# Kernel tuning notes

Measured on AMD Instinct MI355X. Metric: run time of the kernel, lower is better.

## Reference

```python
import jax, jax.numpy as jnp
import numpy as np

B, S, HQ, HKV, D = 2, 1024, 32, 8, 128

def setup_inputs() -> dict:
    key = jax.random.key(0)
    k1, k2, k3 = jax.random.split(key, 3)
    xq = jax.random.normal(k1, (B, S, HQ, D), dtype=jnp.float32)
    xk = jax.random.normal(k2, (B, S, HKV, D), dtype=jnp.float32)
    xv = jax.random.normal(k3, (B, S, HKV, D), dtype=jnp.float32)
    kv_buffer = jnp.zeros((B * S, 2 * HKV, D), dtype=jnp.float32)
    cur_select_index = jnp.arange(B * S, dtype=jnp.int64 if jax.config.read('jax_enable_x64') else jnp.int32)
    return {"xq": xq, "xk": xk, "xv": xv, "kv_buffer": kv_buffer,
            "cur_select_index": cur_select_index}


def reference(xq, xk, xv, kv_buffer, cur_select_index):
    b, s, hq, d = xq.shape
    hkv = xk.shape[2]
    group = hq // hkv

    # --- KV-cache scatter write: kv_buffer[cur_select_index] = cat(k, v) ---
    combined_kv = jnp.concatenate([xk, xv], axis=2).reshape(-1, 2 * hkv, d)
    kv_buffer_new = kv_buffer.at[cur_select_index].set(combined_kv)

    # --- causal flash-style prefill attention (GQA: repeat kv heads) ---
    scale = 1.0 / np.sqrt(d).astype(np.float32)
    k = jnp.repeat(xk, group, axis=2)  # [b, s, hq, d]
    v = jnp.repeat(xv, group, axis=2)

    scores = jnp.einsum('bqhd,bkhd->bhqk', xq, k) * scale  # [b, hq, s, s]
    causal = jnp.tril(jnp.ones((s, s), dtype=bool))
    scores = jnp.where(causal[None, None], scores, jnp.finfo(scores.dtype).min)
    attn = jax.nn.softmax(scores, axis=-1)
    out = jnp.einsum('bhqk,bkhd->bqhd', attn, v)  # [b, s, hq, d]
    out = out.reshape(b, s, hq * d)
    return out, kv_buffer_new
```

## Files before the change

### kernel.cpp

```cpp
#include <hip/hip_runtime.h>
#include <math.h>

#define B_  2
#define S_  1024
#define HQ_ 32
#define HKV_ 8
#define D_  128

typedef __bf16 bf16x8 __attribute__((ext_vector_type(8)));
typedef float  floatx4 __attribute__((ext_vector_type(4)));

static __device__ __forceinline__ unsigned pack2(float hi, float lo) {
    return __builtin_amdgcn_perm(__float_as_uint(hi), __float_as_uint(lo), 0x07060302u);
}

__global__ void kv_scatter_kernel(const float* __restrict__ xk,
                                  const float* __restrict__ xv,
                                  const int* __restrict__ sel,
                                  float* __restrict__ kv_out) {
    const int total = B_ * S_ * 2 * HKV_ * D_ / 4;
    for (int g = blockIdx.x * 256 + threadIdx.x; g < total; g += gridDim.x * 256) {
        const int t      = g >> 9;
        const int within = g & 511;
        const int idx    = sel[t];
        const float4* src = (within < 256)
            ? ((const float4*)(xk + (size_t)t * (HKV_ * D_)) + within)
            : ((const float4*)(xv + (size_t)t * (HKV_ * D_)) + (within - 256));
        ((float4*)(kv_out + (size_t)idx * (2 * HKV_ * D_)))[within] = *src;
    }
}

__global__ __launch_bounds__(256, 2)
void attn_kernel(const float* __restrict__ xq, const float* __restrict__ xk,
                 const float* __restrict__ xv, float* __restrict__ out) {
    const int b    = blockIdx.z;
    const int qt   = (b == 0) ? (int)blockIdx.x : (31 - (int)blockIdx.x);
    const int hk   = blockIdx.y;
    const int tid  = threadIdx.x;
    const int wave = tid >> 6;
    const int lane = tid & 63;
    const int l15  = lane & 15;
    const int quad = lane >> 4;
    const int L    = lane & 31;
    const int hi32 = lane >> 5;
    const int h    = hk * 4 + wave;

    __shared__ __align__(16) unsigned short Kl[2][32][136];
    __shared__ __align__(16) unsigned int   Vp[2][128][16];
    __shared__ __align__(16) unsigned short Pl[4][16][40];

    bf16x8 qf[2][4];
#pragma unroll
    for (int mt = 0; mt < 2; ++mt) {
        const int row = qt * 32 + mt * 16 + l15;
        const float* qp = xq + (((size_t)(b * S_ + row)) * HQ_ + h) * D_ + quad * 8;
#pragma unroll
        for (int ks = 0; ks < 4; ++ks) {
            union { bf16x8 v; unsigned u[4]; } t2;
            const float4 f0 = *(const float4*)(qp + ks * 32);
            const float4 f1 = *(const float4*)(qp + ks * 32 + 4);
            t2.u[0] = pack2(f0.y, f0.x); t2.u[1] = pack2(f0.w, f0.z);
            t2.u[2] = pack2(f1.y, f1.x); t2.u[3] = pack2(f1.w, f1.z);
            qf[mt][ks] = t2.v;
        }
    }

    bf16x8 ones;
    { union { bf16x8 v; unsigned u[4]; } o;
      o.u[0] = o.u[1] = o.u[2] = o.u[3] = 0x3F803F80u; ones = o.v; }

    floatx4 acc[2][8];
    floatx4 lacc[2];
#pragma unroll
    for (int mt = 0; mt < 2; ++mt) {
        lacc[mt] = (floatx4){0.f, 0.f, 0.f, 0.f};
#pragma unroll
        for (int n = 0; n < 8; ++n) acc[mt][n] = (floatx4){0.f, 0.f, 0.f, 0.f};
    }

    const float scale2 = 0.12751741f;

    float4 pk[4], pv[4];
    const int keyw = wave * 2 + hi32;

    auto loads = [&](int t) {
        const size_t base = ((size_t)(b * S_ + t * 32 + keyw) * HKV_ + hk) * D_ + 4 * L;
#pragma unroll
        for (int i = 0; i < 4; ++i) {
            pk[i] = *(const float4*)(xk + base + (size_t)i * 8 * HKV_ * D_);
            pv[i] = *(const float4*)(xv + base + (size_t)i * 8 * HKV_ * D_);
        }
    };

    auto writesLDS = [&](int bi) {
#pragma unroll
        for (int i = 0; i < 4; ++i) {
            const int key = i * 8 + keyw;
            unsigned kw0 = pack2(pk[i].y, pk[i].x), kw1 = pack2(pk[i].w, pk[i].z);
            *(uint2*)&Kl[bi][key][4 * L] = make_uint2(kw0, kw1);
            unsigned D10 = pack2(pv[i].y, pv[i].x), D32 = pack2(pv[i].w, pv[i].z);
            unsigned P10 = (unsigned)__shfl_xor((int)D10, 32);
            unsigned P32 = (unsigned)__shfl_xor((int)D32, 32);
            unsigned w0 = hi32 ? __builtin_amdgcn_perm(D10, P10, 0x07060302u)
                               : __builtin_amdgcn_perm(P10, D10, 0x05040100u);
            unsigned w2 = hi32 ? __builtin_amdgcn_perm(D32, P32, 0x07060302u)
                               : __builtin_amdgcn_perm(P32, D32, 0x05040100u);
            const int col = 4 * ((i + L) & 3) + wave;
            Vp[bi][4 * L + hi32][col]     = w0;
            Vp[bi][4 * L + hi32 + 2][col] = w2;
        }
    };

    auto compute = [&](int bi, bool lastTile) {
#pragma unroll
        for (int mt = 0; mt < 2; ++mt) {
            floatx4 s0 = (floatx4){0.f, 0.f, 0.f, 0.f};
            floatx4 s1 = (floatx4){0.f, 0.f, 0.f, 0.f};
#pragma unroll
            for (int ks = 0; ks < 4; ++ks) {
                bf16x8 kb0 = *(const bf16x8*)&Kl[bi][l15][ks * 32 + quad * 8];
                bf16x8 kb1 = *(const bf16x8*)&Kl[bi][16 + l15][ks * 32 + quad * 8];
                s0 = __builtin_amdgcn_mfma_f32_16x16x32_bf16(qf[mt][ks], kb0, s0, 0, 0, 0);
                s1 = __builtin_amdgcn_mfma_f32_16x16x32_bf16(qf[mt][ks], kb1, s1, 0, 0, 0);
            }
            float p0[4], p1[4];
            if (lastTile) {
                const int rb = mt * 16 + quad * 4;
#pragma unroll
                for (int r = 0; r < 4; ++r) {
                    p0[r] = (l15      <= rb + r) ? __builtin_amdgcn_exp2f(s0[r] * scale2) : 0.f;
                    p1[r] = (l15 + 16 <= rb + r) ? __builtin_amdgcn_exp2f(s1[r] * scale2) : 0.f;
                }
            } else {
#pragma unroll
                for (int r = 0; r < 4; ++r) {
                    p0[r] = __builtin_amdgcn_exp2f(s0[r] * scale2);
                    p1[r] = __builtin_amdgcn_exp2f(s1[r] * scale2);
                }
            }
#pragma unroll
            for (int r = 0; r < 4; ++r) {
                Pl[wave][quad * 4 + r][l15]      = (unsigned short)(__float_as_uint(p0[r]) >> 16);
                Pl[wave][quad * 4 + r][16 + l15] = (unsigned short)(__float_as_uint(p1[r]) >> 16);
            }
            bf16x8 pa = *(const bf16x8*)&Pl[wave][l15][quad * 8];
            lacc[mt] = __builtin_amdgcn_mfma_f32_16x16x32_bf16(pa, ones, lacc[mt], 0, 0, 0);
#pragma unroll
            for (int n = 0; n < 8; ++n) {
                const int d  = n * 16 + l15;
                const int cb = 4 * ((quad + (d >> 2)) & 3);
                bf16x8 vb = *(const bf16x8*)&Vp[bi][d][cb];
                acc[mt][n] = __builtin_amdgcn_mfma_f32_16x16x32_bf16(pa, vb, acc[mt][n], 0, 0, 0);
            }
        }
    };

    const int nkt = qt + 1;
    loads(0);
    writesLDS(0);
    __syncthreads();
    for (int t = 0; t < nkt; ++t) {
        const int bi = t & 1;
        if (t + 1 < nkt) loads(t + 1);
        compute(bi, t == nkt - 1);
        if (t + 1 < nkt) writesLDS(1 - bi);
        __syncthreads();
    }

#pragma unroll
    for (int mt = 0; mt < 2; ++mt) {
#pragma unroll
        for (int r = 0; r < 4; ++r) {
            const float inv = __builtin_amdgcn_rcpf(lacc[mt][r]);
            const int row = qt * 32 + mt * 16 + quad * 4 + r;
            float* op = out + (((size_t)(b * S_ + row)) * HQ_ + h) * D_ + l15;
#pragma unroll
            for (int n = 0; n < 8; ++n) op[n * 16] = acc[mt][n][r] * inv;
        }
    }
}

extern "C" void kernel_launch(void* const* d_in, const int* in_sizes, int n_in,
                              void* d_out, int out_size, void* d_ws, size_t ws_size,
                              hipStream_t stream) {
    const float* xq  = (const float*)d_in[0];
    const float* xk  = (const float*)d_in[1];
    const float* xv  = (const float*)d_in[2];
    const int*   sel = (const int*)d_in[4];

    float* out    = (float*)d_out;
    float* kv_out = out + (size_t)B_ * S_ * HQ_ * D_;

    kv_scatter_kernel<<<dim3(512), dim3(256), 0, stream>>>(xk, xv, sel, kv_out);
    attn_kernel<<<dim3(32, 8, 2), dim3(256), 0, stream>>>(xq, xk, xv, out);
}
```

Measured before the change: 148.0 us.

## Fuse KV scatter into attention launch and split query rows across eight waves

Merges the KV-cache scatter and the attention kernel into one launch, with the first 128 blocks doing the scatter and the rest doing attention. Attention blocks grow to 512 threads (8 waves), each wave handling one 16-row query slab instead of two, which halves per-wave accumulator registers and the per-thread K/V load work. The intent is to remove a launch and the gap between kernels, raise occupancy, and let the scatter overlap with attention. The cost is that each wave now redoes the QK work on its own 16 rows, and the V LDS swizzle is remapped for eight writer waves.

New measurement: 157.3 us. +6.3%, slower.

```diff
diff --git a/kernel.cpp b/kernel.cpp
--- a/kernel.cpp
+++ b/kernel.cpp
@@ -14,45 +14,55 @@
     return __builtin_amdgcn_perm(__float_as_uint(hi), __float_as_uint(lo), 0x07060302u);
 }
 
-__global__ void kv_scatter_kernel(const float* __restrict__ xk,
-                                  const float* __restrict__ xv,
-                                  const int* __restrict__ sel,
-                                  float* __restrict__ kv_out) {
-    const int total = B_ * S_ * 2 * HKV_ * D_ / 4;
-    for (int g = blockIdx.x * 256 + threadIdx.x; g < total; g += gridDim.x * 256) {
-        const int t      = g >> 9;
-        const int within = g & 511;
-        const int idx    = sel[t];
-        const float4* src = (within < 256)
-            ? ((const float4*)(xk + (size_t)t * (HKV_ * D_)) + within)
-            : ((const float4*)(xv + (size_t)t * (HKV_ * D_)) + (within - 256));
-        ((float4*)(kv_out + (size_t)idx * (2 * HKV_ * D_)))[within] = *src;
+#define SCATTER_BLOCKS 128
+#define ATTN_BLOCKS    512
+
+__global__ __launch_bounds__(512, 4)
+void fused_kernel(const float* __restrict__ xq, const float* __restrict__ xk,
+                  const float* __restrict__ xv, const int* __restrict__ sel,
+                  float* __restrict__ out, float* __restrict__ kv_out) {
+    const int lid = blockIdx.x;
+    const int tid = threadIdx.x;
+
+    if (lid < SCATTER_BLOCKS) {
+        int g = lid * 512 + tid;
+        const int stride = SCATTER_BLOCKS * 512;
+#pragma unroll
+        for (int k = 0; k < 16; ++k, g += stride) {
+            const int t      = g >> 9;
+            const int within = g & 511;
+            const int idx    = sel[t];
+            const float4* src = (within < 256)
+                ? ((const float4*)(xk + (size_t)t * (HKV_ * D_)) + within)
+                : ((const float4*)(xv + (size_t)t * (HKV_ * D_)) + (within - 256));
+            ((float4*)(kv_out + (size_t)idx * (2 * HKV_ * D_)))[within] = *src;
+        }
+        return;
     }
-}
 
-__global__ __launch_bounds__(256, 2)
-void attn_kernel(const float* __restrict__ xq, const float* __restrict__ xk,
-                 const float* __restrict__ xv, float* __restrict__ out) {
-    const int b    = blockIdx.z;
-    const int qt   = (b == 0) ? (int)blockIdx.x : (31 - (int)blockIdx.x);
-    const int hk   = blockIdx.y;
-    const int tid  = threadIdx.x;
+    const int wid = lid - SCATTER_BLOCKS;
+    const int hk  = wid & 7;
+    const int j   = wid >> 3;
+    const int b   = j & 1;
+    const int qq  = j >> 1;
+    const int qt  = b ? (31 - qq) : qq;
+
     const int wave = tid >> 6;
     const int lane = tid & 63;
     const int l15  = lane & 15;
     const int quad = lane >> 4;
     const int L    = lane & 31;
     const int hi32 = lane >> 5;
-    const int h    = hk * 4 + wave;
+    const int h    = hk * 4 + (wave & 3);
+    const int mrow = wave >> 2;
 
     __shared__ __align__(16) unsigned short Kl[2][32][136];
     __shared__ __align__(16) unsigned int   Vp[2][128][16];
-    __shared__ __align__(16) unsigned short Pl[4][16][40];
+    __shared__ __align__(16) unsigned short Pl[8][16][40];
 
-    bf16x8 qf[2][4];
-#pragma unroll
-    for (int mt = 0; mt < 2; ++mt) {
-        const int row = qt * 32 + mt * 16 + l15;
+    bf16x8 qf[4];
+    {
+        const int row = qt * 32 + mrow * 16 + l15;
         const float* qp = xq + (((size_t)(b * S_ + row)) * HQ_ + h) * D_ + quad * 8;
 #pragma unroll
         for (int ks = 0; ks < 4; ++ks) {
@@ -61,7 +71,7 @@
             const float4 f1 = *(const float4*)(qp + ks * 32 + 4);
             t2.u[0] = pack2(f0.y, f0.x); t2.u[1] = pack2(f0.w, f0.z);
             t2.u[2] = pack2(f1.y, f1.x); t2.u[3] = pack2(f1.w, f1.z);
-            qf[mt][ks] = t2.v;
+            qf[ks] = t2.v;
         }
     }
 
@@ -69,33 +79,29 @@
     { union { bf16x8 v; unsigned u[4]; } o;
       o.u[0] = o.u[1] = o.u[2] = o.u[3] = 0x3F803F80u; ones = o.v; }
 
-    floatx4 acc[2][8];
-    floatx4 lacc[2];
+    floatx4 acc[8];
+    floatx4 lacc = (floatx4){0.f, 0.f, 0.f, 0.f};
 #pragma unroll
-    for (int mt = 0; mt < 2; ++mt) {
-        lacc[mt] = (floatx4){0.f, 0.f, 0.f, 0.f};
-#pragma unroll
-        for (int n = 0; n < 8; ++n) acc[mt][n] = (floatx4){0.f, 0.f, 0.f, 0.f};
-    }
+    for (int n = 0; n < 8; ++n) acc[n] = (floatx4){0.f, 0.f, 0.f, 0.f};
 
     const float scale2 = 0.12751741f;
 
-    float4 pk[4], pv[4];
+    float4 pk[2], pv[2];
     const int keyw = wave * 2 + hi32;
 
     auto loads = [&](int t) {
         const size_t base = ((size_t)(b * S_ + t * 32 + keyw) * HKV_ + hk) * D_ + 4 * L;
 #pragma unroll
-        for (int i = 0; i < 4; ++i) {
-            pk[i] = *(const float4*)(xk + base + (size_t)i * 8 * HKV_ * D_);
-            pv[i] = *(const float4*)(xv + base + (size_t)i * 8 * HKV_ * D_);
+        for (int i = 0; i < 2; ++i) {
+            pk[i] = *(const float4*)(xk + base + (size_t)i * 16 * HKV_ * D_);
+            pv[i] = *(const float4*)(xv + base + (size_t)i * 16 * HKV_ * D_);
         }
     };
 
     auto writesLDS = [&](int bi) {
 #pragma unroll
-        for (int i = 0; i < 4; ++i) {
-            const int key = i * 8 + keyw;
+        for (int i = 0; i < 2; ++i) {
+            const int key = i * 16 + keyw;
             unsigned kw0 = pack2(pk[i].y, pk[i].x), kw1 = pack2(pk[i].w, pk[i].z);
             *(uint2*)&Kl[bi][key][4 * L] = make_uint2(kw0, kw1);
             unsigned D10 = pack2(pv[i].y, pv[i].x), D32 = pack2(pv[i].w, pv[i].z);
@@ -105,53 +111,51 @@
                                : __builtin_amdgcn_perm(P10, D10, 0x05040100u);
             unsigned w2 = hi32 ? __builtin_amdgcn_perm(D32, P32, 0x07060302u)
                                : __builtin_amdgcn_perm(P32, D32, 0x05040100u);
-            const int col = 4 * ((i + L) & 3) + wave;
+            const int kp  = i * 8 + wave;
+            const int col = 4 * (((kp >> 2) + L) & 3) + (kp & 3);
             Vp[bi][4 * L + hi32][col]     = w0;
             Vp[bi][4 * L + hi32 + 2][col] = w2;
         }
     };
 
     auto compute = [&](int bi, bool lastTile) {
+        floatx4 s0 = (floatx4){0.f, 0.f, 0.f, 0.f};
+        floatx4 s1 = (floatx4){0.f, 0.f, 0.f, 0.f};
 #pragma unroll
-        for (int mt = 0; mt < 2; ++mt) {
-            floatx4 s0 = (floatx4){0.f, 0.f, 0.f, 0.f};
-            floatx4 s1 = (floatx4){0.f, 0.f, 0.f, 0.f};
-#pragma unroll
-            for (int ks = 0; ks < 4; ++ks) {
-                bf16x8 kb0 = *(const bf16x8*)&Kl[bi][l15][ks * 32 + quad * 8];
-                bf16x8 kb1 = *(const bf16x8*)&Kl[bi][16 + l15][ks * 32 + quad * 8];
-                s0 = __builtin_amdgcn_mfma_f32_16x16x32_bf16(qf[mt][ks], kb0, s0, 0, 0, 0);
-                s1 = __builtin_amdgcn_mfma_f32_16x16x32_bf16(qf[mt][ks], kb1, s1, 0, 0, 0);
-            }
-            float p0[4], p1[4];
-            if (lastTile) {
-                const int rb = mt * 16 + quad * 4;
-#pragma unroll
-                for (int r = 0; r < 4; ++r) {
-                    p0[r] = (l15      <= rb + r) ? __builtin_amdgcn_exp2f(s0[r] * scale2) : 0.f;
-                    p1[r] = (l15 + 16 <= rb + r) ? __builtin_amdgcn_exp2f(s1[r] * scale2) : 0.f;
-                }
-            } else {
-#pragma unroll
-                for (int r = 0; r < 4; ++r) {
-                    p0[r] = __builtin_amdgcn_exp2f(s0[r] * scale2);
-                    p1[r] = __builtin_amdgcn_exp2f(s1[r] * scale2);
-                }
-            }
+        for (int ks = 0; ks < 4; ++ks) {
+            bf16x8 kb0 = *(const bf16x8*)&Kl[bi][l15][ks * 32 + quad * 8];
+            bf16x8 kb1 = *(const bf16x8*)&Kl[bi][16 + l15][ks * 32 + quad * 8];
+            s0 = __builtin_amdgcn_mfma_f32_16x16x32_bf16(qf[ks], kb0, s0, 0, 0, 0);
+            s1 = __builtin_amdgcn_mfma_f32_16x16x32_bf16(qf[ks], kb1, s1, 0, 0, 0);
+        }
+        float p0[4], p1[4];
+        const int rb = mrow * 16 + quad * 4;
+        if (lastTile) {
 #pragma unroll
             for (int r = 0; r < 4; ++r) {
-                Pl[wave][quad * 4 + r][l15]      = (unsigned short)(__float_as_uint(p0[r]) >> 16);
-                Pl[wave][quad * 4 + r][16 + l15] = (unsigned short)(__float_as_uint(p1[r]) >> 16);
+                p0[r] = (l15      <= rb + r) ? __builtin_amdgcn_exp2f(s0[r] * scale2) : 0.f;
+                p1[r] = (l15 + 16 <= rb + r) ? __builtin_amdgcn_exp2f(s1[r] * scale2) : 0.f;
             }
-            bf16x8 pa = *(const bf16x8*)&Pl[wave][l15][quad * 8];
-            lacc[mt] = __builtin_amdgcn_mfma_f32_16x16x32_bf16(pa, ones, lacc[mt], 0, 0, 0);
+        } else {
 #pragma unroll
-            for (int n = 0; n < 8; ++n) {
-                const int d  = n * 16 + l15;
-                const int cb = 4 * ((quad + (d >> 2)) & 3);
-                bf16x8 vb = *(const bf16x8*)&Vp[bi][d][cb];
-                acc[mt][n] = __builtin_amdgcn_mfma_f32_16x16x32_bf16(pa, vb, acc[mt][n], 0, 0, 0);
+            for (int r = 0; r < 4; ++r) {
+                p0[r] = __builtin_amdgcn_exp2f(s0[r] * scale2);
+                p1[r] = __builtin_amdgcn_exp2f(s1[r] * scale2);
             }
+        }
+#pragma unroll
+        for (int r = 0; r < 4; ++r) {
+            Pl[wave][quad * 4 + r][l15]      = (unsigned short)(__float_as_uint(p0[r]) >> 16);
+            Pl[wave][quad * 4 + r][16 + l15] = (unsigned short)(__float_as_uint(p1[r]) >> 16);
+        }
+        bf16x8 pa = *(const bf16x8*)&Pl[wave][l15][quad * 8];
+        lacc = __builtin_amdgcn_mfma_f32_16x16x32_bf16(pa, ones, lacc, 0, 0, 0);
+#pragma unroll
+        for (int n = 0; n < 8; ++n) {
+            const int d  = n * 16 + l15;
+            const int cb = 4 * ((quad + (d >> 2)) & 3);
+            bf16x8 vb = *(const bf16x8*)&Vp[bi][d][cb];
+            acc[n] = __builtin_amdgcn_mfma_f32_16x16x32_bf16(pa, vb, acc[n], 0, 0, 0);
         }
     };
 
@@ -168,15 +172,12 @@
     }
 
 #pragma unroll
-    for (int mt = 0; mt < 2; ++mt) {
+    for (int r = 0; r < 4; ++r) {
+        const float inv = __builtin_amdgcn_rcpf(lacc[r]);
+        const int row = qt * 32 + mrow * 16 + quad * 4 + r;
+        float* op = out + (((size_t)(b * S_ + row)) * HQ_ + h) * D_ + l15;
 #pragma unroll
-        for (int r = 0; r < 4; ++r) {
-            const float inv = __builtin_amdgcn_rcpf(lacc[mt][r]);
-            const int row = qt * 32 + mt * 16 + quad * 4 + r;
-            float* op = out + (((size_t)(b * S_ + row)) * HQ_ + h) * D_ + l15;
-#pragma unroll
-            for (int n = 0; n < 8; ++n) op[n * 16] = acc[mt][n][r] * inv;
-        }
+        for (int n = 0; n < 8; ++n) op[n * 16] = acc[n][r] * inv;
     }
 }
 
@@ -191,6 +192,6 @@
     float* out    = (float*)d_out;
     float* kv_out = out + (size_t)B_ * S_ * HQ_ * D_;
 
-    kv_scatter_kernel<<<dim3(512), dim3(256), 0, stream>>>(xk, xv, sel, kv_out);
-    attn_kernel<<<dim3(32, 8, 2), dim3(256), 0, stream>>>(xq, xk, xv, out);
+    fused_kernel<<<dim3(SCATTER_BLOCKS + ATTN_BLOCKS), dim3(512), 0, stream>>>(
+        xq, xk, xv, sel, out, kv_out);
 }
```

## Transpose score MFMA and pass P through ds_bpermute instead of LDS

Applied to the files above, without the earlier changes.

The score MFMA operands are swapped so each lane holds key-major scores. The probability fragment is then rebuilt in registers with ds_bpermute, which replaces the LDS store/load round trip through the Pl buffer. The diagonal tile skips the fully masked upper-key MFMAs for the first row tile. The last tile is peeled out of the loop, and the grid is flattened so heads of the same query tile run in adjacent blocks. This adds eight bpermutes and selects per row tile and changes the block schedule order.

New measurement: 152.1 us. 1.03x slower.

```diff
diff --git a/kernel.cpp b/kernel.cpp
--- a/kernel.cpp
+++ b/kernel.cpp
@@ -33,9 +33,13 @@
 __global__ __launch_bounds__(256, 2)
 void attn_kernel(const float* __restrict__ xq, const float* __restrict__ xk,
                  const float* __restrict__ xv, float* __restrict__ out) {
-    const int b    = blockIdx.z;
-    const int qt   = (b == 0) ? (int)blockIdx.x : (31 - (int)blockIdx.x);
-    const int hk   = blockIdx.y;
+    const int lid = blockIdx.x;
+    const int hk  = lid & 7;
+    const int j   = lid >> 3;
+    const int qq  = j & 31;
+    const int b   = j >> 5;
+    const int qt  = b ? (31 - qq) : qq;
+
     const int tid  = threadIdx.x;
     const int wave = tid >> 6;
     const int lane = tid & 63;
@@ -47,7 +51,6 @@
 
     __shared__ __align__(16) unsigned short Kl[2][32][136];
     __shared__ __align__(16) unsigned int   Vp[2][128][16];
-    __shared__ __align__(16) unsigned short Pl[4][16][40];
 
     bf16x8 qf[2][4];
 #pragma unroll
@@ -116,20 +119,25 @@
         for (int mt = 0; mt < 2; ++mt) {
             floatx4 s0 = (floatx4){0.f, 0.f, 0.f, 0.f};
             floatx4 s1 = (floatx4){0.f, 0.f, 0.f, 0.f};
+            const bool skipHi = lastTile && (mt == 0);
 #pragma unroll
             for (int ks = 0; ks < 4; ++ks) {
                 bf16x8 kb0 = *(const bf16x8*)&Kl[bi][l15][ks * 32 + quad * 8];
-                bf16x8 kb1 = *(const bf16x8*)&Kl[bi][16 + l15][ks * 32 + quad * 8];
-                s0 = __builtin_amdgcn_mfma_f32_16x16x32_bf16(qf[mt][ks], kb0, s0, 0, 0, 0);
-                s1 = __builtin_amdgcn_mfma_f32_16x16x32_bf16(qf[mt][ks], kb1, s1, 0, 0, 0);
+                s0 = __builtin_amdgcn_mfma_f32_16x16x32_bf16(kb0, qf[mt][ks], s0, 0, 0, 0);
+                if (!skipHi) {
+                    bf16x8 kb1 = *(const bf16x8*)&Kl[bi][16 + l15][ks * 32 + quad * 8];
+                    s1 = __builtin_amdgcn_mfma_f32_16x16x32_bf16(kb1, qf[mt][ks], s1, 0, 0, 0);
+                }
             }
             float p0[4], p1[4];
             if (lastTile) {
-                const int rb = mt * 16 + quad * 4;
+                const int mq = mt * 16 + l15;
 #pragma unroll
                 for (int r = 0; r < 4; ++r) {
-                    p0[r] = (l15      <= rb + r) ? __builtin_amdgcn_exp2f(s0[r] * scale2) : 0.f;
-                    p1[r] = (l15 + 16 <= rb + r) ? __builtin_amdgcn_exp2f(s1[r] * scale2) : 0.f;
+                    const int k0 = quad * 4 + r;
+                    p0[r] = (k0 <= mq) ? __builtin_amdgcn_exp2f(s0[r] * scale2) : 0.f;
+                    p1[r] = (!skipHi && k0 + 16 <= mq)
+                            ? __builtin_amdgcn_exp2f(s1[r] * scale2) : 0.f;
                 }
             } else {
 #pragma unroll
@@ -138,12 +146,34 @@
                     p1[r] = __builtin_amdgcn_exp2f(s1[r] * scale2);
                 }
             }
-#pragma unroll
-            for (int r = 0; r < 4; ++r) {
-                Pl[wave][quad * 4 + r][l15]      = (unsigned short)(__float_as_uint(p0[r]) >> 16);
-                Pl[wave][quad * 4 + r][16 + l15] = (unsigned short)(__float_as_uint(p1[r]) >> 16);
-            }
-            bf16x8 pa = *(const bf16x8*)&Pl[wave][l15][quad * 8];
+            unsigned a0 = pack2(p0[1], p0[0]);
+            unsigned a1 = pack2(p0[3], p0[2]);
+            unsigned b0 = pack2(p1[1], p1[0]);
+            unsigned b1 = pack2(p1[3], p1[2]);
+            const int addr0 = (l15 + 16 * ((2 * quad)     & 3)) << 2;
+            const int addr1 = (l15 + 16 * ((2 * quad + 1) & 3)) << 2;
+            union { bf16x8 v; unsigned u[4]; } pau;
+            {
+                unsigned ta = (unsigned)__builtin_amdgcn_ds_bpermute(addr0, (int)a0);
+                unsigned tb = (unsigned)__builtin_amdgcn_ds_bpermute(addr0, (int)b0);
+                pau.u[0] = (quad < 2) ? ta : tb;
+            }
+            {
+                unsigned ta = (unsigned)__builtin_amdgcn_ds_bpermute(addr0, (int)a1);
+                unsigned tb = (unsigned)__builtin_amdgcn_ds_bpermute(addr0, (int)b1);
+                pau.u[1] = (quad < 2) ? ta : tb;
+            }
+            {
+                unsigned ta = (unsigned)__builtin_amdgcn_ds_bpermute(addr1, (int)a0);
+                unsigned tb = (unsigned)__builtin_amdgcn_ds_bpermute(addr1, (int)b0);
+                pau.u[2] = (quad < 2) ? ta : tb;
+            }
+            {
+                unsigned ta = (unsigned)__builtin_amdgcn_ds_bpermute(addr1, (int)a1);
+                unsigned tb = (unsigned)__builtin_amdgcn_ds_bpermute(addr1, (int)b1);
+                pau.u[3] = (quad < 2) ? ta : tb;
+            }
+            bf16x8 pa = pau.v;
             lacc[mt] = __builtin_amdgcn_mfma_f32_16x16x32_bf16(pa, ones, lacc[mt], 0, 0, 0);
 #pragma unroll
             for (int n = 0; n < 8; ++n) {
@@ -159,13 +189,14 @@
     loads(0);
     writesLDS(0);
     __syncthreads();
-    for (int t = 0; t < nkt; ++t) {
+    for (int t = 0; t + 1 < nkt; ++t) {
         const int bi = t & 1;
-        if (t + 1 < nkt) loads(t + 1);
-        compute(bi, t == nkt - 1);
-        if (t + 1 < nkt) writesLDS(1 - bi);
+        loads(t + 1);
+        compute(bi, false);
+        writesLDS(1 - bi);
         __syncthreads();
     }
+    compute((nkt - 1) & 1, true);
 
 #pragma unroll
     for (int mt = 0; mt < 2; ++mt) {
@@ -192,5 +223,5 @@
     float* kv_out = out + (size_t)B_ * S_ * HQ_ * D_;
 
     kv_scatter_kernel<<<dim3(512), dim3(256), 0, stream>>>(xk, xv, sel, kv_out);
-    attn_kernel<<<dim3(32, 8, 2), dim3(256), 0, stream>>>(xq, xk, xv, out);
-}
+    attn_kernel<<<dim3(512), dim3(256), 0, stream>>>(xq, xk, xv, out);
+}
```

## Switch attention to 32x32x16 MFMA with transposed scores kept in registers

Applied to the files above, without the earlier changes.

Reworks the attention inner loop to use 32x32x16 bf16 MFMA, computing S^T = K·Q^T so each lane's score outputs feed directly into the P·V MFMA A operand without staging P through LDS. The row sum is accumulated in registers and reduced with a shuffle instead of an extra MFMA against a ones vector. The V LDS layout is re-swizzled and padded to suit the new operand pattern, the last tile is peeled out of the loop, and the grid is flattened to 1D with heads as the fastest index for better L2 locality. This trades LDS round trips and small-MFMA issue count for higher accumulator register pressure.

Result: slower. 152.6 us (+3.1%).

```diff
diff --git a/kernel.cpp b/kernel.cpp
--- a/kernel.cpp
+++ b/kernel.cpp
@@ -7,8 +7,8 @@
 #define HKV_ 8
 #define D_  128
 
-typedef __bf16 bf16x8 __attribute__((ext_vector_type(8)));
-typedef float  floatx4 __attribute__((ext_vector_type(4)));
+typedef __bf16 bf16x8  __attribute__((ext_vector_type(8)));
+typedef float  floatx16 __attribute__((ext_vector_type(16)));
 
 static __device__ __forceinline__ unsigned pack2(float hi, float lo) {
     return __builtin_amdgcn_perm(__float_as_uint(hi), __float_as_uint(lo), 0x07060302u);
@@ -33,50 +33,47 @@
 __global__ __launch_bounds__(256, 2)
 void attn_kernel(const float* __restrict__ xq, const float* __restrict__ xk,
                  const float* __restrict__ xv, float* __restrict__ out) {
-    const int b    = blockIdx.z;
-    const int qt   = (b == 0) ? (int)blockIdx.x : (31 - (int)blockIdx.x);
-    const int hk   = blockIdx.y;
+    const int lid = blockIdx.x;
+    const int hk  = lid & 7;
+    const int j   = lid >> 3;
+    const int qq  = j & 31;
+    const int b   = j >> 5;
+    const int qt  = b ? (31 - qq) : qq;
+
     const int tid  = threadIdx.x;
     const int wave = tid >> 6;
     const int lane = tid & 63;
-    const int l15  = lane & 15;
-    const int quad = lane >> 4;
+    const int l31  = lane & 31;
     const int L    = lane & 31;
-    const int hi32 = lane >> 5;
+    const int hi   = lane >> 5;
+    const int hi32 = hi;
     const int h    = hk * 4 + wave;
 
     __shared__ __align__(16) unsigned short Kl[2][32][136];
-    __shared__ __align__(16) unsigned int   Vp[2][128][16];
-    __shared__ __align__(16) unsigned short Pl[4][16][40];
+    __shared__ __align__(16) unsigned int   Vp[2][128][20];
+    __shared__ float LxS[4][32];
 
-    bf16x8 qf[2][4];
+    bf16x8 qf[8];
+    {
+        const int row = qt * 32 + l31;
+        const float* qp = xq + (((size_t)(b * S_ + row)) * HQ_ + h) * D_ + hi * 8;
 #pragma unroll
-    for (int mt = 0; mt < 2; ++mt) {
-        const int row = qt * 32 + mt * 16 + l15;
-        const float* qp = xq + (((size_t)(b * S_ + row)) * HQ_ + h) * D_ + quad * 8;
-#pragma unroll
-        for (int ks = 0; ks < 4; ++ks) {
+        for (int s = 0; s < 8; ++s) {
             union { bf16x8 v; unsigned u[4]; } t2;
-            const float4 f0 = *(const float4*)(qp + ks * 32);
-            const float4 f1 = *(const float4*)(qp + ks * 32 + 4);
+            const float4 f0 = *(const float4*)(qp + s * 16);
+            const float4 f1 = *(const float4*)(qp + s * 16 + 4);
             t2.u[0] = pack2(f0.y, f0.x); t2.u[1] = pack2(f0.w, f0.z);
             t2.u[2] = pack2(f1.y, f1.x); t2.u[3] = pack2(f1.w, f1.z);
-            qf[mt][ks] = t2.v;
+            qf[s] = t2.v;
         }
     }
 
-    bf16x8 ones;
-    { union { bf16x8 v; unsigned u[4]; } o;
-      o.u[0] = o.u[1] = o.u[2] = o.u[3] = 0x3F803F80u; ones = o.v; }
-
-    floatx4 acc[2][8];
-    floatx4 lacc[2];
+    floatx16 acc[4];
 #pragma unroll
-    for (int mt = 0; mt < 2; ++mt) {
-        lacc[mt] = (floatx4){0.f, 0.f, 0.f, 0.f};
+    for (int nt = 0; nt < 4; ++nt)
 #pragma unroll
-        for (int n = 0; n < 8; ++n) acc[mt][n] = (floatx4){0.f, 0.f, 0.f, 0.f};
-    }
+        for (int r = 0; r < 16; ++r) acc[nt][r] = 0.f;
+    float lsum = 0.f;
 
     const float scale2 = 0.12751741f;
 
@@ -105,53 +102,52 @@
                                : __builtin_amdgcn_perm(P10, D10, 0x05040100u);
             unsigned w2 = hi32 ? __builtin_amdgcn_perm(D32, P32, 0x07060302u)
                                : __builtin_amdgcn_perm(P32, D32, 0x05040100u);
-            const int col = 4 * ((i + L) & 3) + wave;
+            const int G   = 2 * (i >> 1) + (wave >> 1);
+            const int w   = 2 * (i & 1) + (wave & 1);
+            const int col = 4 * ((G + L) & 3) + w;
             Vp[bi][4 * L + hi32][col]     = w0;
             Vp[bi][4 * L + hi32 + 2][col] = w2;
         }
     };
 
+    const int cb0 = 4 * (((l31 >> 2) + hi)     & 3);
+    const int cb1 = 4 * (((l31 >> 2) + 2 + hi) & 3);
+
     auto compute = [&](int bi, bool lastTile) {
+        floatx16 sA;
 #pragma unroll
-        for (int mt = 0; mt < 2; ++mt) {
-            floatx4 s0 = (floatx4){0.f, 0.f, 0.f, 0.f};
-            floatx4 s1 = (floatx4){0.f, 0.f, 0.f, 0.f};
+        for (int r = 0; r < 16; ++r) sA[r] = 0.f;
 #pragma unroll
-            for (int ks = 0; ks < 4; ++ks) {
-                bf16x8 kb0 = *(const bf16x8*)&Kl[bi][l15][ks * 32 + quad * 8];
-                bf16x8 kb1 = *(const bf16x8*)&Kl[bi][16 + l15][ks * 32 + quad * 8];
-                s0 = __builtin_amdgcn_mfma_f32_16x16x32_bf16(qf[mt][ks], kb0, s0, 0, 0, 0);
-                s1 = __builtin_amdgcn_mfma_f32_16x16x32_bf16(qf[mt][ks], kb1, s1, 0, 0, 0);
+        for (int ss = 0; ss < 8; ++ss) {
+            bf16x8 kb = *(const bf16x8*)&Kl[bi][l31][ss * 16 + hi * 8];
+            sA = __builtin_amdgcn_mfma_f32_32x32x16_bf16(kb, qf[ss], sA, 0, 0, 0);
+        }
+        float p[16];
+        if (lastTile) {
+#pragma unroll
+            for (int r = 0; r < 16; ++r) {
+                const int key = (r & 3) + 8 * (r >> 2) + 4 * hi;
+                p[r] = (key <= l31) ? __builtin_amdgcn_exp2f(sA[r] * scale2) : 0.f;
             }
-            float p0[4], p1[4];
-            if (lastTile) {
-                const int rb = mt * 16 + quad * 4;
+        } else {
 #pragma unroll
-                for (int r = 0; r < 4; ++r) {
-                    p0[r] = (l15      <= rb + r) ? __builtin_amdgcn_exp2f(s0[r] * scale2) : 0.f;
-                    p1[r] = (l15 + 16 <= rb + r) ? __builtin_amdgcn_exp2f(s1[r] * scale2) : 0.f;
-                }
-            } else {
+            for (int r = 0; r < 16; ++r)
+                p[r] = __builtin_amdgcn_exp2f(sA[r] * scale2);
+        }
+        lsum += (((p[0] + p[1]) + (p[2] + p[3])) + ((p[4] + p[5]) + (p[6] + p[7])))
+              + (((p[8] + p[9]) + (p[10] + p[11])) + ((p[12] + p[13]) + (p[14] + p[15])));
+        union { bf16x8 v; unsigned u[4]; } A0, A1;
+        A0.u[0] = pack2(p[1],  p[0]);  A0.u[1] = pack2(p[3],  p[2]);
+        A0.u[2] = pack2(p[5],  p[4]);  A0.u[3] = pack2(p[7],  p[6]);
+        A1.u[0] = pack2(p[9],  p[8]);  A1.u[1] = pack2(p[11], p[10]);
+        A1.u[2] = pack2(p[13], p[12]); A1.u[3] = pack2(p[15], p[14]);
 #pragma unroll
-                for (int r = 0; r < 4; ++r) {
-                    p0[r] = __builtin_amdgcn_exp2f(s0[r] * scale2);
-                    p1[r] = __builtin_amdgcn_exp2f(s1[r] * scale2);
-                }
-            }
-#pragma unroll
-            for (int r = 0; r < 4; ++r) {
-                Pl[wave][quad * 4 + r][l15]      = (unsigned short)(__float_as_uint(p0[r]) >> 16);
-                Pl[wave][quad * 4 + r][16 + l15] = (unsigned short)(__float_as_uint(p1[r]) >> 16);
-            }
-            bf16x8 pa = *(const bf16x8*)&Pl[wave][l15][quad * 8];
-            lacc[mt] = __builtin_amdgcn_mfma_f32_16x16x32_bf16(pa, ones, lacc[mt], 0, 0, 0);
-#pragma unroll
-            for (int n = 0; n < 8; ++n) {
-                const int d  = n * 16 + l15;
-                const int cb = 4 * ((quad + (d >> 2)) & 3);
-                bf16x8 vb = *(const bf16x8*)&Vp[bi][d][cb];
-                acc[mt][n] = __builtin_amdgcn_mfma_f32_16x16x32_bf16(pa, vb, acc[mt][n], 0, 0, 0);
-            }
+        for (int nt = 0; nt < 4; ++nt) {
+            const int d = nt * 32 + l31;
+            bf16x8 vb0 = *(const bf16x8*)&Vp[bi][d][cb0];
+            acc[nt] = __builtin_amdgcn_mfma_f32_32x32x16_bf16(A0.v, vb0, acc[nt], 0, 0, 0);
+            bf16x8 vb1 = *(const bf16x8*)&Vp[bi][d][cb1];
+            acc[nt] = __builtin_amdgcn_mfma_f32_32x32x16_bf16(A1.v, vb1, acc[nt], 0, 0, 0);
         }
     };
 
@@ -159,24 +155,27 @@
     loads(0);
     writesLDS(0);
     __syncthreads();
-    for (int t = 0; t < nkt; ++t) {
+    for (int t = 0; t + 1 < nkt; ++t) {
         const int bi = t & 1;
-        if (t + 1 < nkt) loads(t + 1);
-        compute(bi, t == nkt - 1);
-        if (t + 1 < nkt) writesLDS(1 - bi);
+        loads(t + 1);
+        compute(bi, false);
+        writesLDS(1 - bi);
         __syncthreads();
     }
+    compute((nkt - 1) & 1, true);
 
+    float tot = lsum + __shfl_xor(lsum, 32);
+    LxS[wave][l31] = tot;
+    float inv[16];
 #pragma unroll
-    for (int mt = 0; mt < 2; ++mt) {
+    for (int r = 0; r < 16; ++r)
+        inv[r] = __builtin_amdgcn_rcpf(LxS[wave][(r & 3) + 8 * (r >> 2) + 4 * hi]);
 #pragma unroll
-        for (int r = 0; r < 4; ++r) {
-            const float inv = __builtin_amdgcn_rcpf(lacc[mt][r]);
-            const int row = qt * 32 + mt * 16 + quad * 4 + r;
-            float* op = out + (((size_t)(b * S_ + row)) * HQ_ + h) * D_ + l15;
+    for (int r = 0; r < 16; ++r) {
+        const int row = qt * 32 + (r & 3) + 8 * (r >> 2) + 4 * hi;
+        float* op = out + (((size_t)(b * S_ + row)) * HQ_ + h) * D_ + l31;
 #pragma unroll
-            for (int n = 0; n < 8; ++n) op[n * 16] = acc[mt][n][r] * inv;
-        }
+        for (int nt = 0; nt < 4; ++nt) op[nt * 32] = acc[nt][r] * inv[r];
     }
 }
 
@@ -192,5 +191,5 @@
     float* kv_out = out + (size_t)B_ * S_ * HQ_ * D_;
 
     kv_scatter_kernel<<<dim3(512), dim3(256), 0, stream>>>(xk, xv, sel, kv_out);
-    attn_kernel<<<dim3(32, 8, 2), dim3(256), 0, stream>>>(xq, xk, xv, out);
+    attn_kernel<<<dim3(512), dim3(256), 0, stream>>>(xq, xk, xv, out);
 }
```
